# Optimization experiments

Hardware: AMD Instinct MI355X
Metric: run time of the kernel (lower is better)

Reference implementation:

```python
import jax, jax.numpy as jnp
import numpy as np
import math

NUM_USERS = 100_000
NUM_ITEMS = 200_000
NUM_NODES = NUM_USERS + NUM_ITEMS
EMBED_DIM = 64
N_LAYERS = 3
N_INTERACTIONS = 2_000_000  # -> 4M directed symmetric edges
BATCH = 8192


def setup_inputs() -> dict:
    key = jax.random.key(0)
    ku, ki, ke1, ke2, kb1, kb2, kb3 = jax.random.split(key, 7)
    stdv = 1.0 / math.sqrt(EMBED_DIM)
    user_embedding = jax.random.uniform(ku, (NUM_USERS, EMBED_DIM), jnp.float32, -stdv, stdv)
    item_embedding = jax.random.uniform(ki, (NUM_ITEMS, EMBED_DIM), jnp.float32, -stdv, stdv)

    # random bipartite interactions user <-> item, symmetrized
    e_u = jax.random.randint(ke1, (N_INTERACTIONS,), 0, NUM_USERS, jnp.int32)
    e_i = jax.random.randint(ke2, (N_INTERACTIONS,), 0, NUM_ITEMS, jnp.int32) + NUM_USERS
    edge_src = jnp.concatenate([e_u, e_i])  # [2*N_INTERACTIONS]
    edge_dst = jnp.concatenate([e_i, e_u])

    # symmetric normalization D^{-1/2} A D^{-1/2}
    deg = jax.ops.segment_sum(jnp.ones_like(edge_src, jnp.float32), edge_src,
                              num_segments=NUM_NODES)
    deg = jnp.maximum(deg, 1.0)
    d_inv_sqrt = jax.lax.rsqrt(deg)
    edge_vals = d_inv_sqrt[edge_src] * d_inv_sqrt[edge_dst]

    users = jax.random.randint(kb1, (BATCH,), 0, NUM_USERS, jnp.int64)
    positive_items = jax.random.randint(kb2, (BATCH,), 0, NUM_ITEMS, jnp.int64)
    negative_items = jax.random.randint(kb3, (BATCH,), 0, NUM_ITEMS, jnp.int64)

    return {
        "user_embedding": user_embedding,
        "item_embedding": item_embedding,
        "edge_src": edge_src,
        "edge_dst": edge_dst,
        "edge_vals": edge_vals,
        "users": users,
        "positive_items": positive_items,
        "negative_items": negative_items,
    }


def _computer(user_embedding, item_embedding, edge_src, edge_dst, edge_vals):
    """LightGCN propagation: mean over layer-0..n_layers embeddings."""
    emb = jnp.concatenate([user_embedding, item_embedding], axis=0)  # [N, D]
    acc = emb
    cur = emb
    for _ in range(N_LAYERS):
        # sparse A @ cur via edge gather + segment scatter-add
        msg = edge_vals[:, None] * cur[edge_src]                      # [E, D]
        cur = jax.ops.segment_sum(msg, edge_dst, num_segments=NUM_NODES)
        acc = acc + cur
    light_out = acc / (N_LAYERS + 1)
    return light_out[:NUM_USERS], light_out[NUM_USERS:]


def reference(user_embedding, item_embedding, edge_src, edge_dst, edge_vals,
              users, positive_items, negative_items):
    all_users, all_items = _computer(user_embedding, item_embedding,
                                     edge_src, edge_dst, edge_vals)
    u = all_users[users]                    # [B, D]
    p = all_items[positive_items]           # [B, D]
    n = all_items[negative_items]           # [B, D]
    pos_scores = jnp.sum(u * p, axis=-1)
    neg_scores = jnp.sum(u * n, axis=-1)
    bpr_loss = jnp.mean(jax.nn.softplus(neg_scores - pos_scores))
    return bpr_loss
```

## Files before the change

kernel.cpp:

```cpp
#include <hip/hip_runtime.h>
#include <hip/hip_fp8.h>


#define CDIV(a, b) (((a) + (b) - 1) / (b))

typedef __attribute__((ext_vector_type(8))) unsigned char uchar8;

__device__ __forceinline__ float fp8tof(unsigned char b) {
    __hip_fp8_e4m3 h; h.__x = (__hip_fp8_storage_t)b;
    return (float)h;
}
__device__ __forceinline__ unsigned char ftofp8(float f) {
    __hip_fp8_e4m3 h(f);
    return (unsigned char)h.__x;
}

__device__ __forceinline__ unsigned int dualbits(float f) {
    union { float f; unsigned int u; } c;
    c.f = f;
    unsigned int r = c.u + 0x7FFFu + ((c.u >> 16) & 1u);
    unsigned int b = r >> 16;
    return (b << 16) | b;
}

__global__ void LightGCN_67757404061704_kernel() {}

__global__ void k_mark(unsigned int* __restrict__ out, float v) {
    if (threadIdx.x == 0 && blockIdx.x == 0) out[0] = dualbits(v);
}

__global__ void k_zero_i32(int* __restrict__ p, int n) {
    int t = blockIdx.x * blockDim.x + threadIdx.x;
    if (t < n) p[t] = 0;
}

__global__ void k_zero_f32(float* __restrict__ p, int n) {
    int t = blockIdx.x * blockDim.x + threadIdx.x;
    if (t < n) p[t] = 0.0f;
}

#define BSHIFT 10
#define BNODES 1024
#define EPB_H 4096
#define EPB_A 8192
#define EPT_A (EPB_A / 1024)

__global__ void k_bhist(const int* __restrict__ dst, int* __restrict__ bsize,
                        int E, int NB) {
    __shared__ int h[512];
    for (int i = threadIdx.x; i < NB; i += blockDim.x) h[i] = 0;
    __syncthreads();
    int lo = blockIdx.x * EPB_H;
    int hi = lo + EPB_H; if (hi > E) hi = E;
    for (int k = lo + threadIdx.x; k < hi; k += blockDim.x)
        atomicAdd(&h[dst[k] >> BSHIFT], 1);
    __syncthreads();
    for (int i = threadIdx.x; i < NB; i += blockDim.x)
        if (h[i]) atomicAdd(&bsize[i], h[i]);
}

__global__ void k_bscan(const int* __restrict__ bsize, int* __restrict__ bstart,
                        int* __restrict__ bcur, int NB, int E,
                        int* __restrict__ offs, int N) {
    __shared__ int sm[512];
    int tid = threadIdx.x;
    int v = (tid < NB) ? bsize[tid] : 0;
    sm[tid] = v;
    __syncthreads();
    for (int off = 1; off < 512; off <<= 1) {
        int x = (tid >= off) ? sm[tid - off] : 0;
        __syncthreads();
        sm[tid] += x;
        __syncthreads();
    }
    int excl = sm[tid] - v;
    if (tid <= NB) bstart[tid] = excl;
    if (tid < NB)  bcur[tid] = excl;
    if (tid == 0)  offs[N] = E;
}

__global__ void k_binA(const int* __restrict__ src, const int* __restrict__ dst,
                       int* __restrict__ bcur, unsigned int* __restrict__ staging,
                       int E, int NB) {
    __shared__ int h[512];
    __shared__ int base_s[512];
    int tid = threadIdx.x;
    for (int i = tid; i < NB; i += 1024) h[i] = 0;
    __syncthreads();
    int lo = blockIdx.x * EPB_A;
    int bkt[EPT_A]; int ord[EPT_A]; unsigned int val[EPT_A];
#pragma unroll
    for (int j = 0; j < EPT_A; j++) {
        int k = lo + tid + j * 1024;
        bkt[j] = -1;
        if (k < E) {
            int d = dst[k];
            int s = src[k];
            int b = d >> BSHIFT;
            bkt[j] = b;
            ord[j] = atomicAdd(&h[b], 1);
            val[j] = (unsigned int)s | ((unsigned int)(d & (BNODES - 1)) << 19);
        }
    }
    __syncthreads();
    for (int i = tid; i < NB; i += 1024) {
        int c = h[i];
        base_s[i] = c ? atomicAdd(&bcur[i], c) : 0;
    }
    __syncthreads();
#pragma unroll
    for (int j = 0; j < EPT_A; j++) {
        if (bkt[j] >= 0) staging[base_s[bkt[j]] + ord[j]] = val[j];
    }
}

__global__ void k_binB(const unsigned int* __restrict__ staging,
                       const int* __restrict__ bstart,
                       int* __restrict__ offs, int* __restrict__ edges, int N) {
    int b = blockIdx.x;
    int node0 = b << BSHIFT;
    int nn = N - node0; if (nn > BNODES) nn = BNODES;
    __shared__ int dcnt[BNODES];
    __shared__ int wsum[16];
    int tid = threadIdx.x;
    int lane = tid & 63, wid = tid >> 6;
    dcnt[tid] = 0;
    __syncthreads();
    int s0 = bstart[b], s1 = bstart[b + 1];
    {
        int k = s0 + tid;
        for (; k + 3 * 1024 < s1; k += 4 * 1024) {
            unsigned int r0 = staging[k];
            unsigned int r1 = staging[k + 1024];
            unsigned int r2 = staging[k + 2048];
            unsigned int r3 = staging[k + 3072];
            atomicAdd(&dcnt[r0 >> 19], 1);
            atomicAdd(&dcnt[r1 >> 19], 1);
            atomicAdd(&dcnt[r2 >> 19], 1);
            atomicAdd(&dcnt[r3 >> 19], 1);
        }
        for (; k < s1; k += 1024)
            atomicAdd(&dcnt[staging[k] >> 19], 1);
    }
    __syncthreads();
    int v = dcnt[tid];
    int x = v;
    for (int off = 1; off < 64; off <<= 1) {
        int y = __shfl_up(x, off, 64);
        if (lane >= off) x += y;
    }
    if (lane == 63) wsum[wid] = x;
    __syncthreads();
    if (tid < 16) {
        int s = wsum[tid];
        int xx = s;
        for (int off = 1; off < 16; off <<= 1) {
            int yy = __shfl_up(xx, off, 64);
            if (tid >= off) xx += yy;
        }
        wsum[tid] = xx - s;
    }
    __syncthreads();
    int excl = (x - v) + wsum[wid];
    if (tid < nn) offs[node0 + tid] = s0 + excl;
    dcnt[tid] = excl;
    __syncthreads();
    {
        int k = s0 + tid;
        for (; k + 3 * 1024 < s1; k += 4 * 1024) {
            unsigned int r0 = staging[k];
            unsigned int r1 = staging[k + 1024];
            unsigned int r2 = staging[k + 2048];
            unsigned int r3 = staging[k + 3072];
            int p0 = s0 + atomicAdd(&dcnt[r0 >> 19], 1);
            int p1 = s0 + atomicAdd(&dcnt[r1 >> 19], 1);
            int p2 = s0 + atomicAdd(&dcnt[r2 >> 19], 1);
            int p3 = s0 + atomicAdd(&dcnt[r3 >> 19], 1);
            edges[p0] = (int)(r0 & 0x7FFFFu);
            edges[p1] = (int)(r1 & 0x7FFFFu);
            edges[p2] = (int)(r2 & 0x7FFFFu);
            edges[p3] = (int)(r3 & 0x7FFFFu);
        }
        for (; k < s1; k += 1024) {
            unsigned int r = staging[k];
            int p = s0 + atomicAdd(&dcnt[r >> 19], 1);
            edges[p] = (int)(r & 0x7FFFFu);
        }
    }
}

__global__ void k_hist(const int* __restrict__ dst, int* __restrict__ cnt, int E) {
    int t = blockIdx.x * blockDim.x + threadIdx.x;
    if (t < E) atomicAdd(&cnt[dst[t] + 1], 1);
}

__global__ void k_scan1(const int* __restrict__ data, int* __restrict__ partials, int M) {
    int tid = threadIdx.x;
    int base = blockIdx.x * 2048 + tid * 8;
    int s = 0;
#pragma unroll
    for (int j = 0; j < 8; j++) { int i = base + j; s += (i < M) ? data[i] : 0; }
    __shared__ int sm[256];
    sm[tid] = s; __syncthreads();
    for (int off = 128; off; off >>= 1) {
        if (tid < off) sm[tid] += sm[tid + off];
        __syncthreads();
    }
    if (tid == 0) partials[blockIdx.x] = sm[0];
}

__global__ void k_scan2(int* __restrict__ partials, int nb) {
    if (threadIdx.x == 0 && blockIdx.x == 0) {
        int run = 0;
        for (int b = 0; b < nb; b++) { int v = partials[b]; partials[b] = run; run += v; }
    }
}

__global__ void k_scan3(int* __restrict__ data, const int* __restrict__ partials, int M) {
    int tid = threadIdx.x;
    int base = blockIdx.x * 2048 + tid * 8;
    int v[8]; int s = 0;
#pragma unroll
    for (int j = 0; j < 8; j++) { int i = base + j; v[j] = (i < M) ? data[i] : 0; s += v[j]; }
    __shared__ int sm[256];
    sm[tid] = s; __syncthreads();
    for (int off = 1; off < 256; off <<= 1) {
        int x = (tid >= off) ? sm[tid - off] : 0;
        __syncthreads();
        sm[tid] += x;
        __syncthreads();
    }
    int run = sm[tid] - s + partials[blockIdx.x];
#pragma unroll
    for (int j = 0; j < 8; j++) {
        int i = base + j;
        run += v[j];
        if (i < M) data[i] = run;
    }
}

__global__ void k_copy_i32(const int* __restrict__ a, int* __restrict__ b, int n) {
    int t = blockIdx.x * blockDim.x + threadIdx.x;
    if (t < n) b[t] = a[t];
}

__global__ void k_scatter(const int* __restrict__ src, const int* __restrict__ dst,
                          int* __restrict__ fillpos, int* __restrict__ esrt, int E) {
    int t = blockIdx.x * blockDim.x + threadIdx.x;
    if (t >= E) return;
    int d = dst[t];
    int p = atomicAdd(&fillpos[d], 1);
    esrt[p] = src[t];
}

#define SCALE0 32.0f
#define RENORM 4.0f

__global__ void k_prep(const float4* __restrict__ ue4, const float4* __restrict__ ie4,
                       const int* __restrict__ offs, uchar8* __restrict__ z0,
                       int N, int nu) {
    int t = blockIdx.x * blockDim.x + threadIdx.x;
    int node = t >> 3, lane = t & 7;
    if (node >= N) return;
    int deg = offs[node + 1] - offs[node];
    if (deg < 1) deg = 1;
    float s = SCALE0 * rsqrtf((float)deg);
    const float4* base = (node < nu) ? (ue4 + (size_t)node * 16)
                                     : (ie4 + (size_t)(node - nu) * 16);
    float4 a = base[lane * 2], b = base[lane * 2 + 1];
    uchar8 o;
    o[0] = ftofp8(a.x * s); o[1] = ftofp8(a.y * s);
    o[2] = ftofp8(a.z * s); o[3] = ftofp8(a.w * s);
    o[4] = ftofp8(b.x * s); o[5] = ftofp8(b.y * s);
    o[6] = ftofp8(b.z * s); o[7] = ftofp8(b.w * s);
    z0[(size_t)node * 8 + lane] = o;
}

__global__ void k_spmm_8(const uchar8* __restrict__ zin, uchar8* __restrict__ zout,
                         const int* __restrict__ offs, const int* __restrict__ esrt,
                         int node0, int node1) {
    int t = blockIdx.x * blockDim.x + threadIdx.x;
    int node = node0 + (t >> 3), lane = t & 7;
    if (node >= node1) return;
    int beg = offs[node], end = offs[node + 1];
    float acc[8] = {0.f, 0.f, 0.f, 0.f, 0.f, 0.f, 0.f, 0.f};
    int k = beg;
    for (; k + 8 <= end; k += 8) {
        int s0 = esrt[k],     s1 = esrt[k + 1], s2 = esrt[k + 2], s3 = esrt[k + 3];
        int s4 = esrt[k + 4], s5 = esrt[k + 5], s6 = esrt[k + 6], s7 = esrt[k + 7];
        uchar8 za = zin[(size_t)s0 * 8 + lane];
        uchar8 zb = zin[(size_t)s1 * 8 + lane];
        uchar8 zc = zin[(size_t)s2 * 8 + lane];
        uchar8 zd = zin[(size_t)s3 * 8 + lane];
        uchar8 ze = zin[(size_t)s4 * 8 + lane];
        uchar8 zf = zin[(size_t)s5 * 8 + lane];
        uchar8 zg = zin[(size_t)s6 * 8 + lane];
        uchar8 zh = zin[(size_t)s7 * 8 + lane];
#pragma unroll
        for (int i = 0; i < 8; i++)
            acc[i] += ((fp8tof(za[i]) + fp8tof(zb[i])) +
                       (fp8tof(zc[i]) + fp8tof(zd[i]))) +
                      ((fp8tof(ze[i]) + fp8tof(zf[i])) +
                       (fp8tof(zg[i]) + fp8tof(zh[i])));
    }
    for (; k + 4 <= end; k += 4) {
        int s0 = esrt[k], s1 = esrt[k + 1], s2 = esrt[k + 2], s3 = esrt[k + 3];
        uchar8 za = zin[(size_t)s0 * 8 + lane];
        uchar8 zb = zin[(size_t)s1 * 8 + lane];
        uchar8 zc = zin[(size_t)s2 * 8 + lane];
        uchar8 zd = zin[(size_t)s3 * 8 + lane];
#pragma unroll
        for (int i = 0; i < 8; i++)
            acc[i] += (fp8tof(za[i]) + fp8tof(zb[i])) +
                      (fp8tof(zc[i]) + fp8tof(zd[i]));
    }
    for (; k < end; k++) {
        int s = esrt[k];
        uchar8 z = zin[(size_t)s * 8 + lane];
#pragma unroll
        for (int i = 0; i < 8; i++) acc[i] += fp8tof(z[i]);
    }
    int deg = end - beg;
    float scale = RENORM / (float)(deg < 1 ? 1 : deg);
    uchar8 o;
#pragma unroll
    for (int i = 0; i < 8; i++) o[i] = ftofp8(acc[i] * scale);
    zout[(size_t)node * 8 + lane] = o;
}

__global__ void k_spmm_b(const uchar8* __restrict__ z2, float4* __restrict__ accb,
                         const int* __restrict__ users, const int* __restrict__ pos,
                         const int* __restrict__ neg, const int* __restrict__ offs,
                         const int* __restrict__ esrt, int B, int nu, float invS3) {
    int t = blockIdx.x * blockDim.x + threadIdx.x;
    int r = t >> 3, lane = t & 7;
    if (r >= 3 * B) return;
    int node;
    if (r < B) node = users[r];
    else if (r < 2 * B) node = nu + pos[r - B];
    else node = nu + neg[r - 2 * B];
    int beg = offs[node], end = offs[node + 1];
    float acc[8] = {0.f, 0.f, 0.f, 0.f, 0.f, 0.f, 0.f, 0.f};
    int k = beg;
    for (; k + 8 <= end; k += 8) {
        int s0 = esrt[k],     s1 = esrt[k + 1], s2 = esrt[k + 2], s3 = esrt[k + 3];
        int s4 = esrt[k + 4], s5 = esrt[k + 5], s6 = esrt[k + 6], s7 = esrt[k + 7];
        uchar8 za = z2[(size_t)s0 * 8 + lane];
        uchar8 zb = z2[(size_t)s1 * 8 + lane];
        uchar8 zc = z2[(size_t)s2 * 8 + lane];
        uchar8 zd = z2[(size_t)s3 * 8 + lane];
        uchar8 ze = z2[(size_t)s4 * 8 + lane];
        uchar8 zf = z2[(size_t)s5 * 8 + lane];
        uchar8 zg = z2[(size_t)s6 * 8 + lane];
        uchar8 zh = z2[(size_t)s7 * 8 + lane];
#pragma unroll
        for (int i = 0; i < 8; i++)
            acc[i] += ((fp8tof(za[i]) + fp8tof(zb[i])) +
                       (fp8tof(zc[i]) + fp8tof(zd[i]))) +
                      ((fp8tof(ze[i]) + fp8tof(zf[i])) +
                       (fp8tof(zg[i]) + fp8tof(zh[i])));
    }
    for (; k + 4 <= end; k += 4) {
        int s0 = esrt[k], s1 = esrt[k + 1], s2 = esrt[k + 2], s3 = esrt[k + 3];
        uchar8 za = z2[(size_t)s0 * 8 + lane];
        uchar8 zb = z2[(size_t)s1 * 8 + lane];
        uchar8 zc = z2[(size_t)s2 * 8 + lane];
        uchar8 zd = z2[(size_t)s3 * 8 + lane];
#pragma unroll
        for (int i = 0; i < 8; i++)
            acc[i] += (fp8tof(za[i]) + fp8tof(zb[i])) +
                      (fp8tof(zc[i]) + fp8tof(zd[i]));
    }
    for (; k < end; k++) {
        int s = esrt[k];
        uchar8 z = z2[(size_t)s * 8 + lane];
#pragma unroll
        for (int i = 0; i < 8; i++) acc[i] += fp8tof(z[i]);
    }
    int deg = end - beg;
    if (deg < 1) deg = 1;
    float scale = sqrtf((float)deg) * invS3 * RENORM / (float)deg;
    size_t ai = (size_t)r * 16 + lane * 2;
    float4 a = accb[ai], b = accb[ai + 1];
    a.x += acc[0] * scale; a.y += acc[1] * scale;
    a.z += acc[2] * scale; a.w += acc[3] * scale;
    b.x += acc[4] * scale; b.y += acc[5] * scale;
    b.z += acc[6] * scale; b.w += acc[7] * scale;
    accb[ai] = a; accb[ai + 1] = b;
}

__global__ void k_gather_init(const float4* __restrict__ ue4, const float4* __restrict__ ie4,
                              float4* __restrict__ accb,
                              const int* __restrict__ users, const int* __restrict__ pos,
                              const int* __restrict__ neg, int B, int nu) {
    int t = blockIdx.x * blockDim.x + threadIdx.x;
    int r = t >> 4, lane = t & 15;
    if (r >= 3 * B) return;
    int node;
    if (r < B) node = users[r];
    else if (r < 2 * B) node = nu + pos[r - B];
    else node = nu + neg[r - 2 * B];
    accb[(size_t)r * 16 + lane] = (node < nu) ? ue4[(size_t)node * 16 + lane]
                                              : ie4[(size_t)(node - nu) * 16 + lane];
}

__global__ void k_gather_acc_8(const uchar8* __restrict__ z, float4* __restrict__ accb,
                               const int* __restrict__ users, const int* __restrict__ pos,
                               const int* __restrict__ neg, const int* __restrict__ offs,
                               int B, int nu, float invS) {
    int t = blockIdx.x * blockDim.x + threadIdx.x;
    int r = t >> 3, lane = t & 7;
    if (r >= 3 * B) return;
    int node;
    if (r < B) node = users[r];
    else if (r < 2 * B) node = nu + pos[r - B];
    else node = nu + neg[r - 2 * B];
    int deg = offs[node + 1] - offs[node];
    if (deg < 1) deg = 1;
    float s = sqrtf((float)deg) * invS;
    uchar8 h = z[(size_t)node * 8 + lane];
    size_t ai = (size_t)r * 16 + lane * 2;
    float4 a = accb[ai], b = accb[ai + 1];
    a.x += fp8tof(h[0]) * s; a.y += fp8tof(h[1]) * s;
    a.z += fp8tof(h[2]) * s; a.w += fp8tof(h[3]) * s;
    b.x += fp8tof(h[4]) * s; b.y += fp8tof(h[5]) * s;
    b.z += fp8tof(h[6]) * s; b.w += fp8tof(h[7]) * s;
    accb[ai] = a; accb[ai + 1] = b;
}

__global__ void k_loss(const float* __restrict__ accb, float* __restrict__ lsum, int B) {
    int tid = threadIdx.x;
    int wave = tid >> 6, lane = tid & 63;
    int r = blockIdx.x * 4 + wave;
    float u  = accb[(size_t)r * 64 + lane] * 0.25f;
    float p  = accb[(size_t)(B + r) * 64 + lane] * 0.25f;
    float nv = accb[(size_t)(2 * B + r) * 64 + lane] * 0.25f;
    float pd = u * p, nd = u * nv;
    for (int off = 32; off; off >>= 1) {
        pd += __shfl_down(pd, off, 64);
        nd += __shfl_down(nd, off, 64);
    }
    __shared__ float sm[4];
    if (lane == 0) {
        float x = nd - pd;
        sm[wave] = fmaxf(x, 0.f) + log1pf(expf(-fabsf(x)));
    }
    __syncthreads();
    if (tid == 0) atomicAdd(lsum, sm[0] + sm[1] + sm[2] + sm[3]);
}

__global__ void k_final(const float* __restrict__ lsum, unsigned int* __restrict__ out,
                        float invB) {
    if (threadIdx.x == 0 && blockIdx.x == 0) {
        out[0] = dualbits(lsum[0] * invB);
    }
}

extern "C" void kernel_launch(void* const* d_in, const int* in_sizes, int n_in,
                              void* d_out, int out_size, void* d_ws, size_t ws_size,
                              hipStream_t stream) {
    const float* ue   = (const float*)d_in[0];
    const float* ie   = (const float*)d_in[1];
    const int*   esrc = (const int*)d_in[2];
    const int*   edst = (const int*)d_in[3];
    const int*   usr  = (const int*)d_in[5];
    const int*   pos  = (const int*)d_in[6];
    const int*   neg  = (const int*)d_in[7];

    const int D  = 64;
    const int nu = in_sizes[0] / D;
    const int N  = nu + in_sizes[1] / D;
    const int E  = in_sizes[2];
    const int B  = in_sizes[5];
    (void)n_in; (void)out_size;

    unsigned int* out = (unsigned int*)d_out;

    LightGCN_67757404061704_kernel<<<1, 64, 0, stream>>>();
    k_mark<<<1, 64, 0, stream>>>(out, 5.0f);

    const int NB = CDIV(N, BNODES);

    auto align16 = [](size_t x) { return (x + 15) & ~(size_t)15; };
    size_t need = 0;
    need += 2 * align16((size_t)N * D);
    need += align16((size_t)3 * B * D * sizeof(float));
    need += align16(sizeof(float));
    need += align16((size_t)(N + 1) * sizeof(int));
    need += align16((size_t)N * sizeof(int));
    need += align16((size_t)2048 * sizeof(int));
    need += align16((size_t)512 * sizeof(int));
    need += align16((size_t)513 * sizeof(int));
    need += align16((size_t)512 * sizeof(int));
    need += align16((size_t)E * sizeof(unsigned int));
    need += align16((size_t)E * sizeof(int));
    need += 1024;
    if (d_ws == nullptr || ws_size < need) {
        k_mark<<<1, 64, 0, stream>>>(out, 150.0f);
        return;
    }

    char* w = (char*)d_ws;
    uchar8* z0 = (uchar8*)w;  w += align16((size_t)N * D);
    uchar8* z1 = (uchar8*)w;  w += align16((size_t)N * D);
    float* accb = (float*)w;  w += align16((size_t)3 * B * D * sizeof(float));
    float* lsum = (float*)w;  w += align16(sizeof(float));
    int* offs     = (int*)w;  w += align16((size_t)(N + 1) * sizeof(int));
    int* fillpos  = (int*)w;  w += align16((size_t)N * sizeof(int));
    int* partials = (int*)w;  w += align16((size_t)2048 * sizeof(int));
    int* bsize    = (int*)w;  w += align16((size_t)512 * sizeof(int));
    int* bstart   = (int*)w;  w += align16((size_t)513 * sizeof(int));
    int* bcur     = (int*)w;  w += align16((size_t)512 * sizeof(int));
    unsigned int* staging = (unsigned int*)w; w += align16((size_t)E * sizeof(unsigned int));
    int* esrt     = (int*)w;

    const int BS = 256;

    if (NB <= 511 && N < (1 << 19)) {
        k_zero_i32<<<CDIV(512, BS), BS, 0, stream>>>(bsize, 512);
        k_bhist<<<CDIV(E, EPB_H), BS, 0, stream>>>(edst, bsize, E, NB);
        k_bscan<<<1, 512, 0, stream>>>(bsize, bstart, bcur, NB, E, offs, N);
        k_binA<<<CDIV(E, EPB_A), 1024, 0, stream>>>(esrc, edst, bcur, staging, E, NB);
        k_binB<<<NB, 1024, 0, stream>>>(staging, bstart, offs, esrt, N);
    } else {
        k_zero_i32<<<CDIV(N + 1, BS), BS, 0, stream>>>(offs, N + 1);
        k_hist<<<CDIV(E, BS), BS, 0, stream>>>(edst, offs, E);
        int M = N + 1;
        int nb = CDIV(M, 2048);
        k_scan1<<<nb, BS, 0, stream>>>(offs, partials, M);
        k_scan2<<<1, 64, 0, stream>>>(partials, nb);
        k_scan3<<<nb, BS, 0, stream>>>(offs, partials, M);
        k_copy_i32<<<CDIV(N, BS), BS, 0, stream>>>(offs, fillpos, N);
        k_scatter<<<CDIV(E, BS), BS, 0, stream>>>(esrc, edst, fillpos, esrt, E);
    }

    int pthreads = N * 8;
    k_prep<<<CDIV(pthreads, BS), BS, 0, stream>>>((const float4*)ue, (const float4*)ie,
                                                  offs, z0, N, nu);

    int g16 = 3 * B * 16;
    int g8  = 3 * B * 8;
    k_gather_init<<<CDIV(g16, BS), BS, 0, stream>>>((const float4*)ue, (const float4*)ie,
                                                    (float4*)accb, usr, pos, neg, B, nu);

    int th_items = (N - nu) * 8;
    int th_users = nu * 8;
    uchar8* a = z0; uchar8* b = z1;
    float invS = 1.0f / SCALE0;
    for (int layer = 0; layer < 2; layer++) {
        k_spmm_8<<<CDIV(th_items, BS), BS, 0, stream>>>(a, b, offs, esrt, nu, N);
        k_spmm_8<<<CDIV(th_users, BS), BS, 0, stream>>>(a, b, offs, esrt, 0, nu);
        invS /= RENORM;
        k_gather_acc_8<<<CDIV(g8, BS), BS, 0, stream>>>(b, (float4*)accb,
                                                        usr, pos, neg, offs, B, nu, invS);
        uchar8* tmp = a; a = b; b = tmp;
    }

    k_spmm_b<<<CDIV(g8, BS), BS, 0, stream>>>(a, (float4*)accb, usr, pos, neg,
                                              offs, esrt, B, nu, invS / RENORM);

    k_zero_f32<<<1, 64, 0, stream>>>(lsum, 1);
    k_loss<<<B / 4, BS, 0, stream>>>(accb, lsum, B);
    k_final<<<1, 64, 0, stream>>>(lsum, out, 1.0f / (float)B);
}
```

Before: 423.1 us.

## Use fixed-capacity bucket staging to drop histogram pass and fuse loss finalize

Bucket staging now uses a fixed capacity of CAPB slots per bucket, so binA can append with atomics without a prior histogram and scan. The bhist pass and one launch go away, and the bucket scan runs after binning. The loss finalize is folded into the loss kernel through a last-block-done counter, and the zero and mark launches are merged or removed. The risk is overflow if any bucket holds more than 32768 edges (about 13.7k expected here), and the staging buffer grows to 64 MB.

```diff
diff --git a/kernel.cpp b/kernel.cpp
--- a/kernel.cpp
+++ b/kernel.cpp
@@ -34,50 +34,17 @@
     if (t < n) p[t] = 0;
 }
 
-__global__ void k_zero_f32(float* __restrict__ p, int n) {
-    int t = blockIdx.x * blockDim.x + threadIdx.x;
-    if (t < n) p[t] = 0.0f;
+__global__ void k_zero2(int* __restrict__ bcur, float* __restrict__ lsum) {
+    int t = threadIdx.x;
+    if (t < 512) bcur[t] = 0;
+    if (t == 0) { lsum[0] = 0.0f; ((int*)lsum)[1] = 0; }
 }
 
 #define BSHIFT 10
 #define BNODES 1024
-#define EPB_H 4096
 #define EPB_A 8192
 #define EPT_A (EPB_A / 1024)
-
-__global__ void k_bhist(const int* __restrict__ dst, int* __restrict__ bsize,
-                        int E, int NB) {
-    __shared__ int h[512];
-    for (int i = threadIdx.x; i < NB; i += blockDim.x) h[i] = 0;
-    __syncthreads();
-    int lo = blockIdx.x * EPB_H;
-    int hi = lo + EPB_H; if (hi > E) hi = E;
-    for (int k = lo + threadIdx.x; k < hi; k += blockDim.x)
-        atomicAdd(&h[dst[k] >> BSHIFT], 1);
-    __syncthreads();
-    for (int i = threadIdx.x; i < NB; i += blockDim.x)
-        if (h[i]) atomicAdd(&bsize[i], h[i]);
-}
-
-__global__ void k_bscan(const int* __restrict__ bsize, int* __restrict__ bstart,
-                        int* __restrict__ bcur, int NB, int E,
-                        int* __restrict__ offs, int N) {
-    __shared__ int sm[512];
-    int tid = threadIdx.x;
-    int v = (tid < NB) ? bsize[tid] : 0;
-    sm[tid] = v;
-    __syncthreads();
-    for (int off = 1; off < 512; off <<= 1) {
-        int x = (tid >= off) ? sm[tid - off] : 0;
-        __syncthreads();
-        sm[tid] += x;
-        __syncthreads();
-    }
-    int excl = sm[tid] - v;
-    if (tid <= NB) bstart[tid] = excl;
-    if (tid < NB)  bcur[tid] = excl;
-    if (tid == 0)  offs[N] = E;
-}
+#define CAPB 32768
 
 __global__ void k_binA(const int* __restrict__ src, const int* __restrict__ dst,
                        int* __restrict__ bcur, unsigned int* __restrict__ staging,
@@ -110,12 +77,31 @@
     __syncthreads();
 #pragma unroll
     for (int j = 0; j < EPT_A; j++) {
-        if (bkt[j] >= 0) staging[base_s[bkt[j]] + ord[j]] = val[j];
-    }
+        if (bkt[j] >= 0)
+            staging[(size_t)bkt[j] * CAPB + base_s[bkt[j]] + ord[j]] = val[j];
+    }
+}
+
+__global__ void k_bscan2(const int* __restrict__ bcur, int* __restrict__ bstart,
+                         int NB, int E, int* __restrict__ offs, int N) {
+    __shared__ int sm[512];
+    int tid = threadIdx.x;
+    int v = (tid < NB) ? bcur[tid] : 0;
+    sm[tid] = v;
+    __syncthreads();
+    for (int off = 1; off < 512; off <<= 1) {
+        int x = (tid >= off) ? sm[tid - off] : 0;
+        __syncthreads();
+        sm[tid] += x;
+        __syncthreads();
+    }
+    int excl = sm[tid] - v;
+    if (tid <= NB) bstart[tid] = excl;
+    if (tid == 0)  offs[N] = E;
 }
 
 __global__ void k_binB(const unsigned int* __restrict__ staging,
-                       const int* __restrict__ bstart,
+                       const int* __restrict__ bstart, const int* __restrict__ bcur,
                        int* __restrict__ offs, int* __restrict__ edges, int N) {
     int b = blockIdx.x;
     int node0 = b << BSHIFT;
@@ -126,21 +112,23 @@
     int lane = tid & 63, wid = tid >> 6;
     dcnt[tid] = 0;
     __syncthreads();
-    int s0 = bstart[b], s1 = bstart[b + 1];
+    int sz = bcur[b];
+    size_t sbase = (size_t)b * CAPB;
+    int e0 = bstart[b];
     {
-        int k = s0 + tid;
-        for (; k + 3 * 1024 < s1; k += 4 * 1024) {
-            unsigned int r0 = staging[k];
-            unsigned int r1 = staging[k + 1024];
-            unsigned int r2 = staging[k + 2048];
-            unsigned int r3 = staging[k + 3072];
+        int k = tid;
+        for (; k + 3 * 1024 < sz; k += 4 * 1024) {
+            unsigned int r0 = staging[sbase + k];
+            unsigned int r1 = staging[sbase + k + 1024];
+            unsigned int r2 = staging[sbase + k + 2048];
+            unsigned int r3 = staging[sbase + k + 3072];
             atomicAdd(&dcnt[r0 >> 19], 1);
             atomicAdd(&dcnt[r1 >> 19], 1);
             atomicAdd(&dcnt[r2 >> 19], 1);
             atomicAdd(&dcnt[r3 >> 19], 1);
         }
-        for (; k < s1; k += 1024)
-            atomicAdd(&dcnt[staging[k] >> 19], 1);
+        for (; k < sz; k += 1024)
+            atomicAdd(&dcnt[staging[sbase + k] >> 19], 1);
     }
     __syncthreads();
     int v = dcnt[tid];
@@ -162,28 +150,28 @@
     }
     __syncthreads();
     int excl = (x - v) + wsum[wid];
-    if (tid < nn) offs[node0 + tid] = s0 + excl;
+    if (tid < nn) offs[node0 + tid] = e0 + excl;
     dcnt[tid] = excl;
     __syncthreads();
     {
-        int k = s0 + tid;
-        for (; k + 3 * 1024 < s1; k += 4 * 1024) {
-            unsigned int r0 = staging[k];
-            unsigned int r1 = staging[k + 1024];
-            unsigned int r2 = staging[k + 2048];
-            unsigned int r3 = staging[k + 3072];
-            int p0 = s0 + atomicAdd(&dcnt[r0 >> 19], 1);
-            int p1 = s0 + atomicAdd(&dcnt[r1 >> 19], 1);
-            int p2 = s0 + atomicAdd(&dcnt[r2 >> 19], 1);
-            int p3 = s0 + atomicAdd(&dcnt[r3 >> 19], 1);
+        int k = tid;
+        for (; k + 3 * 1024 < sz; k += 4 * 1024) {
+            unsigned int r0 = staging[sbase + k];
+            unsigned int r1 = staging[sbase + k + 1024];
+            unsigned int r2 = staging[sbase + k + 2048];
+            unsigned int r3 = staging[sbase + k + 3072];
+            int p0 = e0 + atomicAdd(&dcnt[r0 >> 19], 1);
+            int p1 = e0 + atomicAdd(&dcnt[r1 >> 19], 1);
+            int p2 = e0 + atomicAdd(&dcnt[r2 >> 19], 1);
+            int p3 = e0 + atomicAdd(&dcnt[r3 >> 19], 1);
             edges[p0] = (int)(r0 & 0x7FFFFu);
             edges[p1] = (int)(r1 & 0x7FFFFu);
             edges[p2] = (int)(r2 & 0x7FFFFu);
             edges[p3] = (int)(r3 & 0x7FFFFu);
         }
-        for (; k < s1; k += 1024) {
-            unsigned int r = staging[k];
-            int p = s0 + atomicAdd(&dcnt[r >> 19], 1);
+        for (; k < sz; k += 1024) {
+            unsigned int r = staging[sbase + k];
+            int p = e0 + atomicAdd(&dcnt[r >> 19], 1);
             edges[p] = (int)(r & 0x7FFFFu);
         }
     }
@@ -428,7 +416,8 @@
     accb[ai] = a; accb[ai + 1] = b;
 }
 
-__global__ void k_loss(const float* __restrict__ accb, float* __restrict__ lsum, int B) {
+__global__ void k_loss(const float* __restrict__ accb, float* __restrict__ lsum,
+                       unsigned int* __restrict__ out, int B, float invB) {
     int tid = threadIdx.x;
     int wave = tid >> 6, lane = tid & 63;
     int r = blockIdx.x * 4 + wave;
@@ -446,13 +435,15 @@
         sm[wave] = fmaxf(x, 0.f) + log1pf(expf(-fabsf(x)));
     }
     __syncthreads();
-    if (tid == 0) atomicAdd(lsum, sm[0] + sm[1] + sm[2] + sm[3]);
-}
-
-__global__ void k_final(const float* __restrict__ lsum, unsigned int* __restrict__ out,
-                        float invB) {
-    if (threadIdx.x == 0 && blockIdx.x == 0) {
-        out[0] = dualbits(lsum[0] * invB);
+    if (tid == 0) {
+        atomicAdd((float*)lsum, sm[0] + sm[1] + sm[2] + sm[3]);
+        __threadfence();
+        int* done = (int*)lsum + 1;
+        int old = atomicAdd(done, 1);
+        if (old == (int)gridDim.x - 1) {
+            float tot = atomicAdd((float*)lsum, 0.0f);
+            out[0] = dualbits(tot * invB);
+        }
     }
 }
 
@@ -477,7 +468,6 @@
     unsigned int* out = (unsigned int*)d_out;
 
     LightGCN_67757404061704_kernel<<<1, 64, 0, stream>>>();
-    k_mark<<<1, 64, 0, stream>>>(out, 5.0f);
 
     const int NB = CDIV(N, BNODES);
 
@@ -485,14 +475,13 @@
     size_t need = 0;
     need += 2 * align16((size_t)N * D);
     need += align16((size_t)3 * B * D * sizeof(float));
-    need += align16(sizeof(float));
+    need += align16(4 * sizeof(float));
     need += align16((size_t)(N + 1) * sizeof(int));
     need += align16((size_t)N * sizeof(int));
     need += align16((size_t)2048 * sizeof(int));
-    need += align16((size_t)512 * sizeof(int));
     need += align16((size_t)513 * sizeof(int));
     need += align16((size_t)512 * sizeof(int));
-    need += align16((size_t)E * sizeof(unsigned int));
+    need += align16((size_t)512 * CAPB * sizeof(unsigned int));
     need += align16((size_t)E * sizeof(int));
     need += 1024;
     if (d_ws == nullptr || ws_size < need) {
@@ -504,24 +493,23 @@
     uchar8* z0 = (uchar8*)w;  w += align16((size_t)N * D);
     uchar8* z1 = (uchar8*)w;  w += align16((size_t)N * D);
     float* accb = (float*)w;  w += align16((size_t)3 * B * D * sizeof(float));
-    float* lsum = (float*)w;  w += align16(sizeof(float));
+    float* lsum = (float*)w;  w += align16(4 * sizeof(float));
     int* offs     = (int*)w;  w += align16((size_t)(N + 1) * sizeof(int));
     int* fillpos  = (int*)w;  w += align16((size_t)N * sizeof(int));
     int* partials = (int*)w;  w += align16((size_t)2048 * sizeof(int));
-    int* bsize    = (int*)w;  w += align16((size_t)512 * sizeof(int));
     int* bstart   = (int*)w;  w += align16((size_t)513 * sizeof(int));
     int* bcur     = (int*)w;  w += align16((size_t)512 * sizeof(int));
-    unsigned int* staging = (unsigned int*)w; w += align16((size_t)E * sizeof(unsigned int));
+    unsigned int* staging = (unsigned int*)w; w += align16((size_t)512 * CAPB * sizeof(unsigned int));
     int* esrt     = (int*)w;
 
     const int BS = 256;
 
+    k_zero2<<<1, 512, 0, stream>>>(bcur, lsum);
+
     if (NB <= 511 && N < (1 << 19)) {
-        k_zero_i32<<<CDIV(512, BS), BS, 0, stream>>>(bsize, 512);
-        k_bhist<<<CDIV(E, EPB_H), BS, 0, stream>>>(edst, bsize, E, NB);
-        k_bscan<<<1, 512, 0, stream>>>(bsize, bstart, bcur, NB, E, offs, N);
         k_binA<<<CDIV(E, EPB_A), 1024, 0, stream>>>(esrc, edst, bcur, staging, E, NB);
-        k_binB<<<NB, 1024, 0, stream>>>(staging, bstart, offs, esrt, N);
+        k_bscan2<<<1, 512, 0, stream>>>(bcur, bstart, NB, E, offs, N);
+        k_binB<<<NB, 1024, 0, stream>>>(staging, bstart, bcur, offs, esrt, N);
     } else {
         k_zero_i32<<<CDIV(N + 1, BS), BS, 0, stream>>>(offs, N + 1);
         k_hist<<<CDIV(E, BS), BS, 0, stream>>>(edst, offs, E);
@@ -559,7 +547,5 @@
     k_spmm_b<<<CDIV(g8, BS), BS, 0, stream>>>(a, (float4*)accb, usr, pos, neg,
                                               offs, esrt, B, nu, invS / RENORM);
 
-    k_zero_f32<<<1, 64, 0, stream>>>(lsum, 1);
-    k_loss<<<B / 4, BS, 0, stream>>>(accb, lsum, B);
-    k_final<<<1, 64, 0, stream>>>(lsum, out, 1.0f / (float)B);
-}
+    k_loss<<<B / 4, BS, 0, stream>>>(accb, lsum, out, B, 1.0f / (float)B);
+}
```

Measured after the change: 426.1 us. About the same (+0.7%).
